# Performance work log

Hardware: AMD Instinct MI355X
Metric: run time of the kernel (lower is better)

## Reference

```python
import jax, jax.numpy as jnp
import numpy as np

# DH-SFNN: 2 dendritic LIF layers (denri, no tanh, reset-by-subtraction) + leaky readout integrator.
GAMMA = 0.5   # surrogate gradient scale
LENS = 0.5    # surrogate gradient width
VTH = 1.0     # spike threshold
DT = 1.0

@jax.custom_vjp
def spike_fn(x):
    # Heaviside forward, Gaussian surrogate backward (act_fun_adp)
    return (x > 0.0).astype(x.dtype)

def _spike_fwd(x):
    return spike_fn(x), x

def _spike_bwd(x, g):
    sg = GAMMA * jnp.exp(-x * x / (2.0 * LENS * LENS)) / (jnp.sqrt(2.0 * jnp.pi) * LENS)
    return (g * sg,)

spike_fn.defvjp(_spike_fwd, _spike_bwd)

B, T, IN, H, O, K = 256, 250, 700, 256, 20, 4  # batch, time, in_dim, hidden, out_dim, branch
WARMUP = 10


def _branch_mask(rng, out_dim, in_dim, k):
    # Each neuron's k branches see a disjoint random partition of the inputs.
    m = np.zeros((out_dim * k, in_dim), np.float32)
    step = in_dim // k
    for i in range(out_dim):
        perm = rng.permutation(in_dim)
        for j in range(k):
            m[i * k + j, perm[j * step:(j + 1) * step]] = 1.0
    return m


def setup_inputs() -> dict:
    key = jax.random.key(0)
    ks = jax.random.split(key, 12)
    rng = np.random.default_rng(0)
    s1 = 1.0 / np.sqrt(IN)
    s2 = 1.0 / np.sqrt(H)
    # branch-masked dense weights (apply_mask() already baked in)
    W1 = jax.random.uniform(ks[0], (H * K, IN), minval=-s1, maxval=s1) * jnp.asarray(_branch_mask(rng, H, IN, K))
    b1 = jax.random.uniform(ks[1], (H * K,), minval=-s1, maxval=s1)
    tau_n1 = jax.random.uniform(ks[2], (H, K), minval=2.0, maxval=6.0)
    tau_m1 = jax.random.uniform(ks[3], (H,), minval=0.0, maxval=4.0)
    W2 = jax.random.uniform(ks[4], (H * K, H), minval=-s2, maxval=s2) * jnp.asarray(_branch_mask(rng, H, H, K))
    b2 = jax.random.uniform(ks[5], (H * K,), minval=-s2, maxval=s2)
    tau_n2 = jax.random.uniform(ks[6], (H, K), minval=2.0, maxval=6.0)
    tau_m2 = jax.random.uniform(ks[7], (H,), minval=0.0, maxval=4.0)
    Wr = jax.random.uniform(ks[8], (O, H), minval=-s2, maxval=s2)
    br = jax.random.uniform(ks[9], (O,), minval=-s2, maxval=s2)
    tau_mr = jax.random.uniform(ks[10], (O,), minval=0.0, maxval=4.0)
    # sparse binary spike train input (SHD-like)
    x = (jax.random.uniform(ks[11], (B, T, IN)) < 0.1).astype(jnp.float32)
    return dict(x=x, W1=W1, b1=b1, tau_n1=tau_n1, tau_m1=tau_m1,
                W2=W2, b2=b2, tau_n2=tau_n2, tau_m2=tau_m2,
                Wr=Wr, br=br, tau_mr=tau_mr, warmup=WARMUP)


def reference(x, W1, b1, tau_n1, tau_m1, W2, b2, tau_n2, tau_m2, Wr, br, tau_mr, warmup):
    Bb, Tt, _ = x.shape
    beta1 = jax.nn.sigmoid(tau_n1)   # [H,K] dendritic decay
    alpha1 = jax.nn.sigmoid(tau_m1)  # [H]   soma decay
    beta2 = jax.nn.sigmoid(tau_n2)
    alpha2 = jax.nn.sigmoid(tau_m2)
    alphar = jax.nn.sigmoid(tau_mr)  # [O]

    def dense_branch(inp, W, b):
        return (inp @ W.T + b).reshape(inp.shape[0], -1, K)  # [B,H,K]

    def step(carry, xt):
        d1, m1, s1, d2, m2, s2, mr, acc, t = carry
        # layer 1: dendritic filtering then LIF with soft reset
        d1 = beta1 * d1 + (1.0 - beta1) * dense_branch(xt, W1, b1)
        m1 = m1 * alpha1 + (1.0 - alpha1) * DT * d1.sum(-1) - VTH * s1
        s1 = spike_fn(m1 - VTH)
        # layer 2
        d2 = beta2 * d2 + (1.0 - beta2) * dense_branch(s1, W2, b2)
        m2 = m2 * alpha2 + (1.0 - alpha2) * DT * d2.sum(-1) - VTH * s2
        s2 = spike_fn(m2 - VTH)
        # leaky readout integrator
        mr = mr * alphar + (1.0 - alphar) * (s2 @ Wr.T + br)
        acc = acc + jnp.where(t >= warmup, mr, jnp.zeros_like(mr))
        return (d1, m1, s1, d2, m2, s2, mr, acc, t + 1), None

    z = lambda *s: jnp.zeros(s, x.dtype)
    carry0 = (z(Bb, H, K), z(Bb, H), z(Bb, H),
              z(Bb, H, K), z(Bb, H), z(Bb, H),
              z(Bb, O), z(Bb, O), jnp.int32(0))
    carry, _ = jax.lax.scan(step, carry0, jnp.moveaxis(x, 1, 0))
    acc = carry[7]
    return acc / (Tt - warmup)  # readout_mode == 'mean'
```

## Files before the change

kernel.cpp:

```cpp
#include <hip/hip_runtime.h>
#include <hip/hip_bf16.h>

typedef unsigned short us16;
typedef unsigned int u32;

#define B_   256
#define T_   250
#define IN_  700
#define KP_  704
#define H_   256
#define O_   20
#define HK_  1024
#define NPAIR_ (B_ * T_)
#define LDP_ 40
#define CP_  132

typedef __attribute__((ext_vector_type(8))) short short8;
typedef __attribute__((ext_vector_type(4))) float f32x4;

__device__ __forceinline__ float bfbits(unsigned int lo16) {
    union { unsigned int i; float f; } v; v.i = lo16 << 16; return v.f;
}
__device__ __forceinline__ float bflo(unsigned int u) {
    union { unsigned int i; float f; } v; v.i = u << 16; return v.f;
}
__device__ __forceinline__ float bfhi(unsigned int u) {
    union { unsigned int i; float f; } v; v.i = u & 0xffff0000u; return v.f;
}
__device__ __forceinline__ us16 f2bfu(float f) {
    __hip_bfloat16 h = __float2bfloat16(f);
    union { __hip_bfloat16 h; us16 u; } c; c.h = h; return c.u;
}
__device__ __forceinline__ float sigm(float x) { return 1.0f / (1.0f + expf(-x)); }
__device__ __forceinline__ int rfl(int v) { return __builtin_amdgcn_readfirstlane(v); }

__device__ __forceinline__ bool detect_bf16(const us16* __restrict__ taun) {
    int ok = 0;
#pragma unroll
    for (int i = 0; i < 8; i += 2) ok += ((taun[i] >> 8) == 0x40) ? 1 : 0;
    return ok == 4;
}
__device__ __forceinline__ float ldany(const void* __restrict__ p, long i, bool isb) {
    return isb ? bfbits(((const us16*)p)[i]) : ((const float*)p)[i];
}

__device__ __forceinline__ void async_cp16(const us16* g, us16* l) {
    __builtin_amdgcn_global_load_lds(
        (const __attribute__((address_space(1))) u32*)g,
        (__attribute__((address_space(3))) u32*)l, 16, 0, 0);
}

__global__ __launch_bounds__(256) void cvt_rows(
    const void* __restrict__ in, us16* __restrict__ out,
    int R, const us16* __restrict__ taun) {
    const bool isb = detect_bf16(taun);
    const int r = blockIdx.x * 4 + (threadIdx.x >> 6);
    const int l = threadIdx.x & 63;
    if (r >= R) return;
    const long ibase = (long)r * IN_;
    const long obase = (long)r * KP_;
    for (int c = l; c < 176; c += 64) {
        uint2 o;
        if (c < 175) {
            if (isb) {
                o = *(const uint2*)((const us16*)in + ibase + 4 * c);
            } else {
                float4 f = *(const float4*)((const float*)in + ibase + 4 * c);
                o.x = (u32)f2bfu(f.x) | ((u32)f2bfu(f.y) << 16);
                o.y = (u32)f2bfu(f.z) | ((u32)f2bfu(f.w) << 16);
            }
        } else { o.x = 0u; o.y = 0u; }
        *(uint2*)(out + obase + 4 * c) = o;
    }
}

__global__ void transpose_to_bf16(const void* __restrict__ in, us16* __restrict__ out,
                                  int R, int C, const us16* __restrict__ taun) {
    const bool isb = detect_bf16(taun);
    __shared__ us16 tile[32][33];
    int c0 = blockIdx.x * 32, r0 = blockIdx.y * 32;
    int tx = threadIdx.x, ty = threadIdx.y;
#pragma unroll
    for (int j = 0; j < 32; j += 8) {
        int r = r0 + ty + j, c = c0 + tx;
        if (r < R && c < C) tile[ty + j][tx] = f2bfu(ldany(in, (long)r * C + c, isb));
    }
    __syncthreads();
#pragma unroll
    for (int j = 0; j < 32; j += 8) {
        int c = c0 + ty + j, r = r0 + tx;
        if (c < C && r < R) out[(long)c * R + r] = tile[tx][ty + j];
    }
}

__global__ __launch_bounds__(256) void gemm_bf(
    const us16* __restrict__ Xb, const us16* __restrict__ W1b,
    us16* __restrict__ Apre)
{
    __shared__ __align__(16) us16 smem[128 * CP_];
    us16* As = smem;
    us16* Bs = smem + 128 * 64;

    const int L  = blockIdx.x;
    const int mt = (L & 7) + ((L >> 6) << 3);
    const int nt = (L >> 3) & 7;
    if (mt >= NPAIR_ / 128) return;
    const int m0 = mt * 128, n0 = nt * 128;

    const int tid  = threadIdx.x;
    const int lane = tid & 63;
    const int w    = tid >> 6;
    const int wr   = w >> 1, wc = w & 1;
    const int l16  = lane & 15, quad = lane >> 4;

    const int rr    = lane >> 3;
    const int ccsw  = ((lane & 7) ^ rr) * 8;
    const us16* xg[4]; const us16* wg[4];
    us16* asl[4]; us16* bsl[4];
#pragma unroll
    for (int i = 0; i < 4; ++i) {
        const int blkrow = (w * 4 + i) * 8;
        xg[i]  = Xb  + (long)(m0 + blkrow + rr) * KP_ + ccsw;
        wg[i]  = W1b + (long)(n0 + blkrow + rr) * KP_ + ccsw;
        asl[i] = As + (w * 4 + i) * 512;
        bsl[i] = Bs + (w * 4 + i) * 512;
    }

    f32x4 acc[4][4];
#pragma unroll
    for (int i = 0; i < 4; ++i)
#pragma unroll
        for (int j = 0; j < 4; ++j) acc[i][j] = (f32x4){0.f, 0.f, 0.f, 0.f};

    const int sw = l16 & 7;
    int aoff0[4], aoff1[4], boff0[4], boff1[4];
#pragma unroll
    for (int i = 0; i < 4; ++i) {
        const int ar = wr * 64 + i * 16 + l16;
        const int br = wc * 64 + i * 16 + l16;
        aoff0[i] = ar * 64 + ((quad ^ sw) << 3);
        aoff1[i] = ar * 64 + (((quad + 4) ^ sw) << 3);
        boff0[i] = br * 64 + ((quad ^ sw) << 3);
        boff1[i] = br * 64 + (((quad + 4) ^ sw) << 3);
    }

    for (int s = 0; s < 11; ++s) {
        const int kb = s * 64;
        __syncthreads();
#pragma unroll
        for (int i = 0; i < 4; ++i) async_cp16(xg[i] + kb, asl[i]);
#pragma unroll
        for (int i = 0; i < 4; ++i) async_cp16(wg[i] + kb, bsl[i]);
        __syncthreads();

        short8 af[4][2], bfv[4][2];
#pragma unroll
        for (int i = 0; i < 4; ++i) {
            af[i][0]  = *(const short8*)(As + aoff0[i]);
            af[i][1]  = *(const short8*)(As + aoff1[i]);
            bfv[i][0] = *(const short8*)(Bs + boff0[i]);
            bfv[i][1] = *(const short8*)(Bs + boff1[i]);
        }
#pragma unroll
        for (int h = 0; h < 2; ++h)
#pragma unroll
            for (int i = 0; i < 4; ++i)
#pragma unroll
                for (int j = 0; j < 4; ++j)
                    acc[i][j] = __builtin_amdgcn_mfma_f32_16x16x32_bf16(
                        af[i][h], bfv[j][h], acc[i][j], 0, 0, 0);
    }

    __syncthreads();
#pragma unroll
    for (int i = 0; i < 4; ++i)
#pragma unroll
        for (int j = 0; j < 4; ++j)
#pragma unroll
            for (int r = 0; r < 4; ++r)
                smem[(wr * 64 + i * 16 + quad * 4 + r) * CP_ +
                     (wc * 64 + j * 16 + l16)] = f2bfu(acc[i][j][r]);
    __syncthreads();
    for (int r2 = 0; r2 < 32; ++r2) {
        const int row = w * 32 + r2;
        const u32 v = *(const u32*)(smem + row * CP_ + lane * 2);
        *(u32*)(Apre + (long)(m0 + row) * HK_ + n0 + lane * 2) = v;
    }
}

__global__ __launch_bounds__(256) void dhsfnn_pc(
    const us16* __restrict__ Apre,
    const void* __restrict__ b1,  const void* __restrict__ tau_n1,
    const void* __restrict__ tau_m1,
    const void* __restrict__ b2,  const void* __restrict__ tau_n2,
    const void* __restrict__ tau_m2,
    const void* __restrict__ Wr,  const void* __restrict__ br,
    const void* __restrict__ tau_mr,
    const us16* __restrict__ W2T,
    const int* __restrict__ warmup_p,
    void* __restrict__ out)
{
    __shared__ __align__(16) us16 ring[2][16 * HK_];

    const int tid  = threadIdx.x;
    const int lane = tid & 63;
    const int w    = tid >> 6;
    const int b    = blockIdx.x;
    const bool isb = detect_bf16((const us16*)tau_n1);
    const int wu   = *warmup_p;

    const us16* apb = Apre + (long)b * T_ * HK_;

    {
        const uint4* src = (const uint4*)apb;
        uint4* dst = (uint4*)ring[0];
        for (int k = tid; k < 16 * 128; k += 256) dst[k] = src[k];
    }

    float be1[16], cb1[16], ce1[16], be2[16], cb2[16], ce2[16], d1[16], d2[16];
#pragma unroll
    for (int e = 0; e < 16; ++e) {
        const long gi = (e < 8) ? ((long)lane * 8 + e) : (512 + (long)lane * 8 + e - 8);
        const float t1 = sigm(ldany(tau_n1, gi, isb));
        be1[e] = t1; ce1[e] = 1.f - t1; cb1[e] = ce1[e] * ldany(b1, gi, isb);
        const float t2 = sigm(ldany(tau_n2, gi, isb));
        be2[e] = t2; ce2[e] = 1.f - t2; cb2[e] = ce2[e] * ldany(b2, gi, isb);
        d1[e] = 0.f; d2[e] = 0.f;
    }
    float al1[4], al2[4], m1[4], s1[4], m2[4], s2[4];
#pragma unroll
    for (int j = 0; j < 4; ++j) {
        const int n = (j < 2) ? (2 * lane + j) : (128 + 2 * lane + (j - 2));
        al1[j] = sigm(ldany(tau_m1, n, isb));
        al2[j] = sigm(ldany(tau_m2, n, isb));
        m1[j] = 0.f; s1[j] = 0.f; m2[j] = 0.f; s2[j] = 0.f;
    }
    float alr = 0.f, brv = 0.f;
    if (lane < O_) { alr = sigm(ldany(tau_mr, lane, isb)); brv = ldany(br, lane, isb); }
    float mrv = 0.f, accO = 0.f;

    __syncthreads();

    for (int c = 0; c < 16; ++c) {
        const int t0 = c * 16;
        const int nst = (T_ - t0 < 16) ? (T_ - t0) : 16;

        if (w != 0) {
            if (c + 1 < 16) {
                const int t1c = (c + 1) * 16;
                const int nn  = ((T_ - t1c < 16) ? (T_ - t1c) : 16) * 128;
                const uint4* src = (const uint4*)(apb + (long)t1c * HK_);
                uint4* dst = (uint4*)ring[(c + 1) & 1];
                for (int k = tid - 64; k < nn; k += 192) dst[k] = src[k];
            }
        } else {
            const us16* rb = ring[c & 1];
            uint4 cLo = *(const uint4*)(rb + lane * 8);
            uint4 cHi = *(const uint4*)(rb + 512 + lane * 8);
            for (int q = 0; q < nst; ++q) {
                uint4 nLo = cLo, nHi = cHi;
                if (q + 1 < nst) {
                    nLo = *(const uint4*)(rb + (q + 1) * HK_ + lane * 8);
                    nHi = *(const uint4*)(rb + (q + 1) * HK_ + 512 + lane * 8);
                }
                const int t = t0 + q;
                float a[16];
                a[0]=bflo(cLo.x);  a[1]=bfhi(cLo.x);  a[2]=bflo(cLo.y);  a[3]=bfhi(cLo.y);
                a[4]=bflo(cLo.z);  a[5]=bfhi(cLo.z);  a[6]=bflo(cLo.w);  a[7]=bfhi(cLo.w);
                a[8]=bflo(cHi.x);  a[9]=bfhi(cHi.x);  a[10]=bflo(cHi.y); a[11]=bfhi(cHi.y);
                a[12]=bflo(cHi.z); a[13]=bfhi(cHi.z); a[14]=bflo(cHi.w); a[15]=bfhi(cHi.w);

#pragma unroll
                for (int e = 0; e < 16; ++e)
                    d1[e] = be1[e] * d1[e] + cb1[e] + ce1[e] * a[e];

                unsigned long long bal1[4];
#pragma unroll
                for (int j = 0; j < 4; ++j) {
                    const float s = (d1[j*4+0] + d1[j*4+1]) + (d1[j*4+2] + d1[j*4+3]);
                    m1[j] = m1[j] * al1[j] + (1.f - al1[j]) * s - s1[j];
                    s1[j] = (m1[j] > 1.0f) ? 1.f : 0.f;
                    bal1[j] = __ballot(s1[j] > 0.f);
                }

                if ((bal1[0] | bal1[1] | bal1[2] | bal1[3]) != 0ull) {
                    float g[16];
#pragma unroll
                    for (int e = 0; e < 16; ++e) g[e] = 0.f;
                    for (int j2 = 0; j2 < 4; ++j2) {
                        unsigned long long mm = bal1[j2];
                        while (mm) {
                            const int i = __ffsll(mm) - 1; mm &= mm - 1;
                            const int n = (j2 < 2) ? (2 * i + j2) : (128 + 2 * i + (j2 - 2));
                            const us16* wv = W2T + ((long)n << 10);
                            const uint4 wl = *(const uint4*)(wv + lane * 8);
                            const uint4 wh = *(const uint4*)(wv + 512 + lane * 8);
                            g[0]+=bflo(wl.x);  g[1]+=bfhi(wl.x);  g[2]+=bflo(wl.y);  g[3]+=bfhi(wl.y);
                            g[4]+=bflo(wl.z);  g[5]+=bfhi(wl.z);  g[6]+=bflo(wl.w);  g[7]+=bfhi(wl.w);
                            g[8]+=bflo(wh.x);  g[9]+=bfhi(wh.x);  g[10]+=bflo(wh.y); g[11]+=bfhi(wh.y);
                            g[12]+=bflo(wh.z); g[13]+=bfhi(wh.z); g[14]+=bflo(wh.w); g[15]+=bfhi(wh.w);
                        }
                    }
#pragma unroll
                    for (int e = 0; e < 16; ++e)
                        d2[e] = be2[e] * d2[e] + cb2[e] + ce2[e] * g[e];
                } else {
#pragma unroll
                    for (int e = 0; e < 16; ++e)
                        d2[e] = be2[e] * d2[e] + cb2[e];
                }

                unsigned long long bal2[4];
#pragma unroll
                for (int j = 0; j < 4; ++j) {
                    const float s = (d2[j*4+0] + d2[j*4+1]) + (d2[j*4+2] + d2[j*4+3]);
                    m2[j] = m2[j] * al2[j] + (1.f - al2[j]) * s - s2[j];
                    s2[j] = (m2[j] > 1.0f) ? 1.f : 0.f;
                    bal2[j] = __ballot(s2[j] > 0.f);
                }

                if (lane < O_) {
                    float sum = brv;
                    if ((bal2[0] | bal2[1] | bal2[2] | bal2[3]) != 0ull) {
                        for (int j2 = 0; j2 < 4; ++j2) {
                            unsigned long long mm = bal2[j2];
                            while (mm) {
                                const int i = __ffsll(mm) - 1; mm &= mm - 1;
                                const int n = (j2 < 2) ? (2 * i + j2) : (128 + 2 * i + (j2 - 2));
                                sum += ldany(Wr, (long)lane * H_ + n, isb);
                            }
                        }
                    }
                    mrv = alr * mrv + (1.f - alr) * sum;
                    if (t >= wu) accO += mrv;
                }
                cLo = nLo; cHi = nHi;
            }
        }
        __syncthreads();
    }

    if (w == 0 && lane < O_) {
        const float res = accO / (float)(T_ - wu);
        if (isb) ((us16*)out)[b * O_ + lane] = f2bfu(res);
        else     ((float*)out)[b * O_ + lane] = res;
    }
}

#define GA_LOAD(S, AV, BV) do {                                               \
    const int k0_ = (S) * 32 + half16;                                        \
    if (k0_ + 16 <= IN_) {                                                    \
        if (isb) {                                                            \
            const us16* pa_ = (const us16*)X  + arow + k0_;                   \
            const us16* pb_ = (const us16*)W1 + brow + k0_;                   \
            uint2 a0_ = *(const uint2*)pa_,        a1_ = *(const uint2*)(pa_ + 4);  \
            uint2 a2_ = *(const uint2*)(pa_ + 8),  a3_ = *(const uint2*)(pa_ + 12); \
            uint2 b0_ = *(const uint2*)pb_,        b1_ = *(const uint2*)(pb_ + 4);  \
            uint2 b2_ = *(const uint2*)(pb_ + 8),  b3_ = *(const uint2*)(pb_ + 12); \
            AV[0]=a0_.x; AV[1]=a0_.y; AV[2]=a1_.x; AV[3]=a1_.y;               \
            AV[4]=a2_.x; AV[5]=a2_.y; AV[6]=a3_.x; AV[7]=a3_.y;               \
            BV[0]=b0_.x; BV[1]=b0_.y; BV[2]=b1_.x; BV[3]=b1_.y;               \
            BV[4]=b2_.x; BV[5]=b2_.y; BV[6]=b3_.x; BV[7]=b3_.y;               \
        } else {                                                              \
            const float* pa_ = (const float*)X  + arow + k0_;                 \
            const float* pb_ = (const float*)W1 + brow + k0_;                 \
            float4 fa0_ = *(const float4*)pa_,        fa1_ = *(const float4*)(pa_ + 4);  \
            float4 fa2_ = *(const float4*)(pa_ + 8),  fa3_ = *(const float4*)(pa_ + 12); \
            float4 fb0_ = *(const float4*)pb_,        fb1_ = *(const float4*)(pb_ + 4);  \
            float4 fb2_ = *(const float4*)(pb_ + 8),  fb3_ = *(const float4*)(pb_ + 12); \
            AV[0] = (unsigned)f2bfu(fa0_.x) | ((unsigned)f2bfu(fa0_.y) << 16); \
            AV[1] = (unsigned)f2bfu(fa0_.z) | ((unsigned)f2bfu(fa0_.w) << 16); \
            AV[2] = (unsigned)f2bfu(fa1_.x) | ((unsigned)f2bfu(fa1_.y) << 16); \
            AV[3] = (unsigned)f2bfu(fa1_.z) | ((unsigned)f2bfu(fa1_.w) << 16); \
            AV[4] = (unsigned)f2bfu(fa2_.x) | ((unsigned)f2bfu(fa2_.y) << 16); \
            AV[5] = (unsigned)f2bfu(fa2_.z) | ((unsigned)f2bfu(fa2_.w) << 16); \
            AV[6] = (unsigned)f2bfu(fa3_.x) | ((unsigned)f2bfu(fa3_.y) << 16); \
            AV[7] = (unsigned)f2bfu(fa3_.z) | ((unsigned)f2bfu(fa3_.w) << 16); \
            BV[0] = (unsigned)f2bfu(fb0_.x) | ((unsigned)f2bfu(fb0_.y) << 16); \
            BV[1] = (unsigned)f2bfu(fb0_.z) | ((unsigned)f2bfu(fb0_.w) << 16); \
            BV[2] = (unsigned)f2bfu(fb1_.x) | ((unsigned)f2bfu(fb1_.y) << 16); \
            BV[3] = (unsigned)f2bfu(fb1_.z) | ((unsigned)f2bfu(fb1_.w) << 16); \
            BV[4] = (unsigned)f2bfu(fb2_.x) | ((unsigned)f2bfu(fb2_.y) << 16); \
            BV[5] = (unsigned)f2bfu(fb2_.z) | ((unsigned)f2bfu(fb2_.w) << 16); \
            BV[6] = (unsigned)f2bfu(fb3_.x) | ((unsigned)f2bfu(fb3_.y) << 16); \
            BV[7] = (unsigned)f2bfu(fb3_.z) | ((unsigned)f2bfu(fb3_.w) << 16); \
        }                                                                     \
    } else {                                                                  \
        _Pragma("unroll")                                                     \
        for (int e_ = 0; e_ < 8; ++e_) { AV[e_] = 0u; BV[e_] = 0u; }          \
        _Pragma("unroll")                                                     \
        for (int e_ = 0; e_ < 16; ++e_) {                                     \
            int k_ = k0_ + e_;                                                \
            if (k_ < IN_) {                                                   \
                unsigned va_ = (unsigned)f2bfu(ldany(X,  arow + k_, isb));    \
                unsigned vb_ = (unsigned)f2bfu(ldany(W1, brow + k_, isb));    \
                AV[e_ >> 1] |= va_ << ((e_ & 1) * 16);                        \
                BV[e_ >> 1] |= vb_ << ((e_ & 1) * 16);                        \
            }                                                                 \
        }                                                                     \
    }                                                                         \
} while (0)

#define GA_STORE(AV, BV) do {                                                 \
    uint4 u0_; u0_.x = AV[0]; u0_.y = AV[1]; u0_.z = AV[2]; u0_.w = AV[3];    \
    uint4 u1_; u1_.x = AV[4]; u1_.y = AV[5]; u1_.z = AV[6]; u1_.w = AV[7];    \
    uint4 v0_; v0_.x = BV[0]; v0_.y = BV[1]; v0_.z = BV[2]; v0_.w = BV[3];    \
    uint4 v1_; v1_.x = BV[4]; v1_.y = BV[5]; v1_.z = BV[6]; v1_.w = BV[7];    \
    *(uint4*)asw       = u0_; *(uint4*)(asw + 8) = u1_;                       \
    *(uint4*)bsw       = v0_; *(uint4*)(bsw + 8) = v1_;                       \
} while (0)

#define GA_MFMA() do {                                                        \
    short8 af_[4], bf_[4];                                                    \
    _Pragma("unroll")                                                         \
    for (int i_ = 0; i_ < 4; ++i_) af_[i_] = *(const short8*)(As + aoff[i_]); \
    _Pragma("unroll")                                                         \
    for (int j_ = 0; j_ < 4; ++j_) bf_[j_] = *(const short8*)(Bs + boff[j_]); \
    _Pragma("unroll")                                                         \
    for (int i_ = 0; i_ < 4; ++i_)                                            \
        _Pragma("unroll")                                                     \
        for (int j_ = 0; j_ < 4; ++j_)                                        \
            acc[i_][j_] = __builtin_amdgcn_mfma_f32_16x16x32_bf16(            \
                af_[i_], bf_[j_], acc[i_][j_], 0, 0, 0);                      \
} while (0)

__global__ __launch_bounds__(256) void gemm_apre(
    const void* __restrict__ X, const void* __restrict__ W1,
    const us16* __restrict__ taun, us16* __restrict__ Apre)
{
    const bool isb = detect_bf16(taun);
    __shared__ __align__(16) us16 As[128 * LDP_];
    __shared__ __align__(16) us16 Bs[128 * LDP_];

    const int L  = blockIdx.x;
    const int mt = (L & 7) + ((L >> 6) << 3);
    const int nt = (L >> 3) & 7;
    if (mt >= NPAIR_ / 128) return;
    const int m0 = mt * 128, n0 = nt * 128;

    const int tid  = threadIdx.x;
    const int lane = tid & 63;
    const int w    = tid >> 6;
    const int wr   = w >> 1, wc = w & 1;
    const int l16  = lane & 15, quad = lane >> 4;
    const int ra   = tid >> 1;
    const int half16 = (tid & 1) * 16;

    f32x4 acc[4][4];
#pragma unroll
    for (int i = 0; i < 4; ++i)
#pragma unroll
        for (int j = 0; j < 4; ++j) acc[i][j] = (f32x4){0.f, 0.f, 0.f, 0.f};

    int aoff[4], boff[4];
#pragma unroll
    for (int i = 0; i < 4; ++i) {
        aoff[i] = (wr * 64 + i * 16 + l16) * LDP_ + quad * 8;
        boff[i] = (wc * 64 + i * 16 + l16) * LDP_ + quad * 8;
    }

    const long arow = (long)(m0 + ra) * IN_;
    const long brow = (long)(n0 + ra) * IN_;
    us16* asw = As + ra * LDP_ + half16;
    us16* bsw = Bs + ra * LDP_ + half16;

    unsigned av0[8], bv0[8], av1[8], bv1[8];
    GA_LOAD(0, av0, bv0);

    for (int ss = 0; ss < 11; ++ss) {
        __syncthreads();
        GA_STORE(av0, bv0);
        __syncthreads();
        GA_LOAD(2 * ss + 1, av1, bv1);
        GA_MFMA();
        __syncthreads();
        GA_STORE(av1, bv1);
        __syncthreads();
        if (ss < 10) GA_LOAD(2 * ss + 2, av0, bv0);
        GA_MFMA();
    }

#pragma unroll
    for (int i = 0; i < 4; ++i) {
#pragma unroll
        for (int j = 0; j < 4; ++j) {
            const int gm = m0 + wr * 64 + i * 16 + quad * 4;
            const int gn = n0 + wc * 64 + j * 16 + l16;
            us16* op = Apre + (long)gm * HK_ + gn;
#pragma unroll
            for (int r = 0; r < 4; ++r)
                op[(long)r * HK_] = f2bfu(acc[i][j][r]);
        }
    }
}

__global__ __launch_bounds__(64) void dhsfnn_wave(
    const us16* __restrict__ Apre,
    const void* __restrict__ b1,  const void* __restrict__ tau_n1,
    const void* __restrict__ tau_m1,
    const void* __restrict__ b2,  const void* __restrict__ tau_n2,
    const void* __restrict__ tau_m2,
    const void* __restrict__ Wr,  const void* __restrict__ br,
    const void* __restrict__ tau_mr,
    const us16* __restrict__ W2T,
    const int* __restrict__ warmup_p,
    void* __restrict__ out)
{
    const int lane = threadIdx.x;
    const int b    = blockIdx.x;
    const bool isb = detect_bf16((const us16*)tau_n1);
    const int wu   = *warmup_p;

    float be1[16], cb1[16], be2[16], cb2[16], d1[16], d2[16];
#pragma unroll
    for (int e = 0; e < 16; ++e) {
        const long gi = (long)lane * 16 + e;
        const float t1 = sigm(ldany(tau_n1, gi, isb));
        be1[e] = t1; cb1[e] = (1.f - t1) * ldany(b1, gi, isb);
        const float t2 = sigm(ldany(tau_n2, gi, isb));
        be2[e] = t2; cb2[e] = (1.f - t2) * ldany(b2, gi, isb);
        d1[e] = 0.f; d2[e] = 0.f;
    }
    float al1[4], al2[4], m1[4], s1[4], m2[4], s2[4];
#pragma unroll
    for (int j = 0; j < 4; ++j) {
        al1[j] = sigm(ldany(tau_m1, lane * 4 + j, isb));
        al2[j] = sigm(ldany(tau_m2, lane * 4 + j, isb));
        m1[j] = 0.f; s1[j] = 0.f; m2[j] = 0.f; s2[j] = 0.f;
    }
    float alr = 0.f, brv = 0.f;
    if (lane < O_) { alr = sigm(ldany(tau_mr, lane, isb)); brv = ldany(br, lane, isb); }
    float mrv = 0.f, accO = 0.f;

    const us16* ap = Apre + (long)b * T_ * HK_ + lane * 16;

    auto wstep = [&](int t, uint4 lo, uint4 hi) {
        float a[16];
        a[0]=bflo(lo.x);  a[1]=bfhi(lo.x);  a[2]=bflo(lo.y);  a[3]=bfhi(lo.y);
        a[4]=bflo(lo.z);  a[5]=bfhi(lo.z);  a[6]=bflo(lo.w);  a[7]=bfhi(lo.w);
        a[8]=bflo(hi.x);  a[9]=bfhi(hi.x);  a[10]=bflo(hi.y); a[11]=bfhi(hi.y);
        a[12]=bflo(hi.z); a[13]=bfhi(hi.z); a[14]=bflo(hi.w); a[15]=bfhi(hi.w);
#pragma unroll
        for (int e = 0; e < 16; ++e)
            d1[e] = be1[e] * d1[e] + cb1[e] + (1.f - be1[e]) * a[e];
        unsigned long long bal1[4];
#pragma unroll
        for (int j = 0; j < 4; ++j) {
            const float s = (d1[j*4+0] + d1[j*4+1]) + (d1[j*4+2] + d1[j*4+3]);
            m1[j] = m1[j] * al1[j] + (1.f - al1[j]) * s - s1[j];
            s1[j] = (m1[j] > 1.0f) ? 1.f : 0.f;
            bal1[j] = __ballot(s1[j] > 0.f);
        }
        if ((bal1[0] | bal1[1] | bal1[2] | bal1[3]) != 0ull) {
            float g[16];
#pragma unroll
            for (int e = 0; e < 16; ++e) g[e] = 0.f;
            for (int j2 = 0; j2 < 4; ++j2) {
                unsigned long long mm = bal1[j2];
                while (mm) {
                    const int i = __ffsll(mm) - 1; mm &= mm - 1;
                    const us16* wv = W2T + ((long)(i * 4 + j2) << 10) + lane * 16;
                    const uint4 wl = *(const uint4*)wv;
                    const uint4 wh = *(const uint4*)(wv + 8);
                    g[0]+=bflo(wl.x);  g[1]+=bfhi(wl.x);  g[2]+=bflo(wl.y);  g[3]+=bfhi(wl.y);
                    g[4]+=bflo(wl.z);  g[5]+=bfhi(wl.z);  g[6]+=bflo(wl.w);  g[7]+=bfhi(wl.w);
                    g[8]+=bflo(wh.x);  g[9]+=bfhi(wh.x);  g[10]+=bflo(wh.y); g[11]+=bfhi(wh.y);
                    g[12]+=bflo(wh.z); g[13]+=bfhi(wh.z); g[14]+=bflo(wh.w); g[15]+=bfhi(wh.w);
                }
            }
#pragma unroll
            for (int e = 0; e < 16; ++e)
                d2[e] = be2[e] * d2[e] + cb2[e] + (1.f - be2[e]) * g[e];
        } else {
#pragma unroll
            for (int e = 0; e < 16; ++e)
                d2[e] = be2[e] * d2[e] + cb2[e];
        }
        unsigned long long bal2[4];
#pragma unroll
        for (int j = 0; j < 4; ++j) {
            const float s = (d2[j*4+0] + d2[j*4+1]) + (d2[j*4+2] + d2[j*4+3]);
            m2[j] = m2[j] * al2[j] + (1.f - al2[j]) * s - s2[j];
            s2[j] = (m2[j] > 1.0f) ? 1.f : 0.f;
            bal2[j] = __ballot(s2[j] > 0.f);
        }
        if (lane < O_) {
            float sum = brv;
            if ((bal2[0] | bal2[1] | bal2[2] | bal2[3]) != 0ull) {
                for (int j2 = 0; j2 < 4; ++j2) {
                    unsigned long long mm = bal2[j2];
                    while (mm) {
                        const int i = __ffsll(mm) - 1; mm &= mm - 1;
                        sum += ldany(Wr, (long)lane * H_ + (i * 4 + j2), isb);
                    }
                }
            }
            mrv = alr * mrv + (1.f - alr) * sum;
            if (t >= wu) accO += mrv;
        }
    };

    uint4 q0a = *(const uint4*)(ap);
    uint4 q0b = *(const uint4*)(ap + 8);
    uint4 q1a = *(const uint4*)(ap + HK_);
    uint4 q1b = *(const uint4*)(ap + HK_ + 8);
    uint4 q2a = *(const uint4*)(ap + 2 * HK_);
    uint4 q2b = *(const uint4*)(ap + 2 * HK_ + 8);
    uint4 q3a = *(const uint4*)(ap + 3 * HK_);
    uint4 q3b = *(const uint4*)(ap + 3 * HK_ + 8);

    int t = 0;
    for (int it = 0; it < 62; ++it) {
        wstep(t + 0, q0a, q0b);
        q0a = *(const uint4*)(ap + (long)(t + 4) * HK_);
        q0b = *(const uint4*)(ap + (long)(t + 4) * HK_ + 8);
        wstep(t + 1, q1a, q1b);
        if (t + 5 < T_) {
            q1a = *(const uint4*)(ap + (long)(t + 5) * HK_);
            q1b = *(const uint4*)(ap + (long)(t + 5) * HK_ + 8);
        }
        wstep(t + 2, q2a, q2b);
        if (t + 6 < T_) {
            q2a = *(const uint4*)(ap + (long)(t + 6) * HK_);
            q2b = *(const uint4*)(ap + (long)(t + 6) * HK_ + 8);
        }
        wstep(t + 3, q3a, q3b);
        if (t + 7 < T_) {
            q3a = *(const uint4*)(ap + (long)(t + 7) * HK_);
            q3b = *(const uint4*)(ap + (long)(t + 7) * HK_ + 8);
        }
        t += 4;
    }
    wstep(248, q0a, q0b);
    wstep(249, q1a, q1b);

    if (lane < O_) {
        const float res = accO / (float)(T_ - wu);
        if (isb) ((us16*)out)[b * O_ + lane] = f2bfu(res);
        else     ((float*)out)[b * O_ + lane] = res;
    }
}

__global__ __launch_bounds__(256) void dhsfnn_fb(
    const void* __restrict__ x,  const void* __restrict__ W1,
    const void* __restrict__ b1, const void* __restrict__ tau_n1,
    const void* __restrict__ tau_m1,
    const void* __restrict__ W2, const void* __restrict__ b2,
    const void* __restrict__ tau_n2, const void* __restrict__ tau_m2,
    const void* __restrict__ Wr, const void* __restrict__ br,
    const void* __restrict__ tau_mr,
    const int* __restrict__ warmup_p,
    void* __restrict__ out)
{
    __shared__ us16 list1[1024];
    __shared__ us16 list2[256];
    __shared__ us16 list3[256];
    __shared__ int n1s, n2s, n3s;

    const int tid = threadIdx.x;
    const int b   = blockIdx.x;
    const int h   = tid;
    const bool isb = detect_bf16((const us16*)tau_n1);
    const int wu  = *warmup_p;

    const float be1_0 = sigm(ldany(tau_n1, 4 * h + 0, isb));
    const float be1_1 = sigm(ldany(tau_n1, 4 * h + 1, isb));
    const float be1_2 = sigm(ldany(tau_n1, 4 * h + 2, isb));
    const float be1_3 = sigm(ldany(tau_n1, 4 * h + 3, isb));
    const float bi1_0 = ldany(b1, 4 * h + 0, isb), bi1_1 = ldany(b1, 4 * h + 1, isb);
    const float bi1_2 = ldany(b1, 4 * h + 2, isb), bi1_3 = ldany(b1, 4 * h + 3, isb);
    const float al1 = sigm(ldany(tau_m1, h, isb));
    const float be2_0 = sigm(ldany(tau_n2, 4 * h + 0, isb));
    const float be2_1 = sigm(ldany(tau_n2, 4 * h + 1, isb));
    const float be2_2 = sigm(ldany(tau_n2, 4 * h + 2, isb));
    const float be2_3 = sigm(ldany(tau_n2, 4 * h + 3, isb));
    const float bi2_0 = ldany(b2, 4 * h + 0, isb), bi2_1 = ldany(b2, 4 * h + 1, isb);
    const float bi2_2 = ldany(b2, 4 * h + 2, isb), bi2_3 = ldany(b2, 4 * h + 3, isb);
    const float al2 = sigm(ldany(tau_m2, h, isb));
    float alr = 0.f, brv = 0.f;
    if (h < O_) { alr = sigm(ldany(tau_mr, h, isb)); brv = ldany(br, h, isb); }

    float d1_0 = 0.f, d1_1 = 0.f, d1_2 = 0.f, d1_3 = 0.f, m1v = 0.f, s1f = 0.f;
    float d2_0 = 0.f, d2_1 = 0.f, d2_2 = 0.f, d2_3 = 0.f, m2v = 0.f, s2f = 0.f;
    float mrv = 0.f, accO = 0.f;

    const long xbase = (long)b * T_ * IN_;
    float xv0 = ldany(x, xbase + tid, isb);
    float xv1 = ldany(x, xbase + tid + 256, isb);
    float xv2 = (tid + 512 < IN_) ? ldany(x, xbase + tid + 512, isb) : 0.f;

    for (int t = 0; t < T_; ++t) {
        const bool p0 = xv0 != 0.f, p1 = xv1 != 0.f, p2 = xv2 != 0.f;
        if (t + 1 < T_) {
            const long nbx = xbase + (long)(t + 1) * IN_;
            xv0 = ldany(x, nbx + tid, isb);
            xv1 = ldany(x, nbx + tid + 256, isb);
            xv2 = (tid + 512 < IN_) ? ldany(x, nbx + tid + 512, isb) : 0.f;
        }
        __syncthreads();
        if (tid == 0) { n1s = 0; n2s = 0; n3s = 0; }
        __syncthreads();
        if (p0) { int p = atomicAdd(&n1s, 1); list1[p & 1023] = (us16)tid; }
        if (p1) { int p = atomicAdd(&n1s, 1); list1[p & 1023] = (us16)(tid + 256); }
        if (p2) { int p = atomicAdd(&n1s, 1); list1[p & 1023] = (us16)(tid + 512); }
        __syncthreads();
        int n1 = n1s; n1 = (n1 < 1024) ? n1 : 1024;

        float a0 = 0.f, a1 = 0.f, a2 = 0.f, a3 = 0.f;
#pragma unroll 2
        for (int idx = 0; idx < n1; ++idx) {
            int i = rfl((int)list1[idx]);
            i = (i < IN_) ? i : (IN_ - 1);
            long r = (long)(h * 4) * IN_ + i;
            a0 += ldany(W1, r, isb);
            a1 += ldany(W1, r + IN_, isb);
            a2 += ldany(W1, r + 2 * IN_, isb);
            a3 += ldany(W1, r + 3 * IN_, isb);
        }
        d1_0 = be1_0 * d1_0 + (1.f - be1_0) * (bi1_0 + a0);
        d1_1 = be1_1 * d1_1 + (1.f - be1_1) * (bi1_1 + a1);
        d1_2 = be1_2 * d1_2 + (1.f - be1_2) * (bi1_2 + a2);
        d1_3 = be1_3 * d1_3 + (1.f - be1_3) * (bi1_3 + a3);
        m1v = m1v * al1 + (1.f - al1) * (d1_0 + d1_1 + d1_2 + d1_3) - s1f;
        s1f = (m1v > 1.0f) ? 1.f : 0.f;

        if (s1f > 0.f) { int p = atomicAdd(&n2s, 1); list2[p & 255] = (us16)tid; }
        __syncthreads();
        int n2 = n2s; n2 = (n2 < 256) ? n2 : 256;

        a0 = 0.f; a1 = 0.f; a2 = 0.f; a3 = 0.f;
#pragma unroll 2
        for (int idx = 0; idx < n2; ++idx) {
            int i = rfl((int)list2[idx]);
            i = (i < H_) ? i : (H_ - 1);
            long r = (long)(h * 4) * H_ + i;
            a0 += ldany(W2, r, isb);
            a1 += ldany(W2, r + H_, isb);
            a2 += ldany(W2, r + 2 * H_, isb);
            a3 += ldany(W2, r + 3 * H_, isb);
        }
        d2_0 = be2_0 * d2_0 + (1.f - be2_0) * (bi2_0 + a0);
        d2_1 = be2_1 * d2_1 + (1.f - be2_1) * (bi2_1 + a1);
        d2_2 = be2_2 * d2_2 + (1.f - be2_2) * (bi2_2 + a2);
        d2_3 = be2_3 * d2_3 + (1.f - be2_3) * (bi2_3 + a3);
        m2v = m2v * al2 + (1.f - al2) * (d2_0 + d2_1 + d2_2 + d2_3) - s2f;
        s2f = (m2v > 1.0f) ? 1.f : 0.f;

        if (s2f > 0.f) { int p = atomicAdd(&n3s, 1); list3[p & 255] = (us16)tid; }
        __syncthreads();
        int n3 = n3s; n3 = (n3 < 256) ? n3 : 256;

        if (h < O_) {
            float sum = brv;
            for (int idx = 0; idx < n3; ++idx) {
                int j = (int)list3[idx];
                j = (j < H_) ? j : (H_ - 1);
                sum += ldany(Wr, (long)h * H_ + j, isb);
            }
            mrv = alr * mrv + (1.f - alr) * sum;
            if (t >= wu) accO += mrv;
        }
    }
    if (h < O_) {
        float res = accO / (float)(T_ - wu);
        if (isb) ((us16*)out)[b * O_ + h] = f2bfu(res);
        else     ((float*)out)[b * O_ + h] = res;
    }
}

extern "C" void kernel_launch(void* const* d_in, const int* in_sizes, int n_in,
                              void* d_out, int out_size, void* d_ws, size_t ws_size,
                              hipStream_t stream) {
    const void* x      = d_in[0];
    const void* W1     = d_in[1];
    const void* b1     = d_in[2];
    const void* tau_n1 = d_in[3];
    const void* tau_m1 = d_in[4];
    const void* W2     = d_in[5];
    const void* b2     = d_in[6];
    const void* tau_n2 = d_in[7];
    const void* tau_m2 = d_in[8];
    const void* Wr     = d_in[9];
    const void* br     = d_in[10];
    const void* tau_mr = d_in[11];
    const int*  warmup = (const int*)d_in[12];

    const size_t w2t_bytes  = (size_t)H_ * HK_ * 2;
    const size_t xbf_bytes  = (size_t)NPAIR_ * KP_ * 2;
    const size_t w1b_bytes  = (size_t)HK_ * KP_ * 2;
    const size_t apre_bytes = (size_t)NPAIR_ * HK_ * 2;

    const bool tier0 = (d_ws != nullptr &&
                        ws_size >= w2t_bytes + xbf_bytes + w1b_bytes + apre_bytes);
    const bool tier1 = (d_ws != nullptr && ws_size >= w2t_bytes + apre_bytes);

    dim3 blk(32, 8);
    if (tier0) {
        us16* W2T  = (us16*)d_ws;
        us16* Xbf  = (us16*)((char*)d_ws + w2t_bytes);
        us16* W1bf = (us16*)((char*)d_ws + w2t_bytes + xbf_bytes);
        us16* Apre = (us16*)((char*)d_ws + w2t_bytes + xbf_bytes + w1b_bytes);
        cvt_rows<<<NPAIR_ / 4, 256, 0, stream>>>(x, Xbf, NPAIR_, (const us16*)tau_n1);
        cvt_rows<<<HK_ / 4, 256, 0, stream>>>(W1, W1bf, HK_, (const us16*)tau_n1);
        transpose_to_bf16<<<dim3((H_ + 31) / 32, (HK_ + 31) / 32), blk, 0, stream>>>(
            W2, W2T, HK_, H_, (const us16*)tau_n1);
        gemm_bf<<<4096, 256, 0, stream>>>(Xbf, W1bf, Apre);
        dhsfnn_pc<<<B_, 256, 0, stream>>>(
            Apre, b1, tau_n1, tau_m1, b2, tau_n2, tau_m2,
            Wr, br, tau_mr, W2T, warmup, d_out);
    } else if (tier1) {
        us16* W2T  = (us16*)d_ws;
        us16* Apre = (us16*)((char*)d_ws + w2t_bytes);
        transpose_to_bf16<<<dim3((H_ + 31) / 32, (HK_ + 31) / 32), blk, 0, stream>>>(
            W2, W2T, HK_, H_, (const us16*)tau_n1);
        gemm_apre<<<4096, 256, 0, stream>>>(x, W1, (const us16*)tau_n1, Apre);
        dhsfnn_wave<<<B_, 64, 0, stream>>>(
            Apre, b1, tau_n1, tau_m1, b2, tau_n2, tau_m2,
            Wr, br, tau_mr, W2T, warmup, d_out);
    } else {
        dhsfnn_fb<<<B_, 256, 0, stream>>>(x, W1, b1, tau_n1, tau_m1,
                                          W2, b2, tau_n2, tau_m2,
                                          Wr, br, tau_mr, warmup, d_out);
    }
}
```

Before: 481.7 us.

## Enlarge GEMM M-tile to 256 rows and merge input conversion kernels

The bf16 GEMM for the layer-1 pre-activations now computes 256x128 tiles instead of 128x128, halving the grid and reusing each loaded W1 slice across twice as many rows. The epilogue writes the result through shared memory in two passes. The separate x and W1 conversion launches are merged into one kernel to save a launch. The change raises accumulator register pressure (32 f32x4 per thread), which may lower occupancy.

```diff
diff --git a/kernel.cpp b/kernel.cpp
--- a/kernel.cpp
+++ b/kernel.cpp
@@ -50,15 +50,21 @@
         (__attribute__((address_space(3))) u32*)l, 16, 0, 0);
 }
 
-__global__ __launch_bounds__(256) void cvt_rows(
-    const void* __restrict__ in, us16* __restrict__ out,
-    int R, const us16* __restrict__ taun) {
+__global__ __launch_bounds__(256) void cvt_rows2(
+    const void* __restrict__ xin, const void* __restrict__ w1in,
+    us16* __restrict__ xout, us16* __restrict__ w1out,
+    const us16* __restrict__ taun) {
     const bool isb = detect_bf16(taun);
     const int r = blockIdx.x * 4 + (threadIdx.x >> 6);
     const int l = threadIdx.x & 63;
-    if (r >= R) return;
-    const long ibase = (long)r * IN_;
-    const long obase = (long)r * KP_;
+    const void* in; us16* out; long ibase, obase;
+    if (r < NPAIR_) {
+        in = xin;  out = xout;  ibase = (long)r * IN_; obase = (long)r * KP_;
+    } else {
+        const int r2 = r - NPAIR_;
+        if (r2 >= HK_) return;
+        in = w1in; out = w1out; ibase = (long)r2 * IN_; obase = (long)r2 * KP_;
+    }
     for (int c = l; c < 176; c += 64) {
         uint2 o;
         if (c < 175) {
@@ -97,15 +103,15 @@
     const us16* __restrict__ Xb, const us16* __restrict__ W1b,
     us16* __restrict__ Apre)
 {
-    __shared__ __align__(16) us16 smem[128 * CP_];
+    __shared__ __align__(16) us16 smem[24576];
     us16* As = smem;
-    us16* Bs = smem + 128 * 64;
+    us16* Bs = smem + 16384;
 
     const int L  = blockIdx.x;
     const int mt = (L & 7) + ((L >> 6) << 3);
     const int nt = (L >> 3) & 7;
-    if (mt >= NPAIR_ / 128) return;
-    const int m0 = mt * 128, n0 = nt * 128;
+    if (mt >= NPAIR_ / 256) return;
+    const int m0 = mt * 256, n0 = nt * 128;
 
     const int tid  = threadIdx.x;
     const int lane = tid & 63;
@@ -113,78 +119,91 @@
     const int wr   = w >> 1, wc = w & 1;
     const int l16  = lane & 15, quad = lane >> 4;
 
-    const int rr    = lane >> 3;
-    const int ccsw  = ((lane & 7) ^ rr) * 8;
-    const us16* xg[4]; const us16* wg[4];
-    us16* asl[4]; us16* bsl[4];
+    const int rr   = lane >> 3;
+    const int ccsw = ((lane & 7) ^ rr) * 8;
+    const us16* xg[8]; us16* asl[8];
+    const us16* wg[4]; us16* bsl[4];
+#pragma unroll
+    for (int i = 0; i < 8; ++i) {
+        const int g = w * 8 + i;
+        xg[i]  = Xb + (long)(m0 + g * 8 + rr) * KP_ + ccsw;
+        asl[i] = As + g * 512;
+    }
 #pragma unroll
     for (int i = 0; i < 4; ++i) {
-        const int blkrow = (w * 4 + i) * 8;
-        xg[i]  = Xb  + (long)(m0 + blkrow + rr) * KP_ + ccsw;
-        wg[i]  = W1b + (long)(n0 + blkrow + rr) * KP_ + ccsw;
-        asl[i] = As + (w * 4 + i) * 512;
-        bsl[i] = Bs + (w * 4 + i) * 512;
-    }
-
-    f32x4 acc[4][4];
-#pragma unroll
-    for (int i = 0; i < 4; ++i)
+        const int g = w * 4 + i;
+        wg[i]  = W1b + (long)(n0 + g * 8 + rr) * KP_ + ccsw;
+        bsl[i] = Bs + g * 512;
+    }
+
+    f32x4 acc[8][4];
+#pragma unroll
+    for (int i = 0; i < 8; ++i)
 #pragma unroll
         for (int j = 0; j < 4; ++j) acc[i][j] = (f32x4){0.f, 0.f, 0.f, 0.f};
 
     const int sw = l16 & 7;
-    int aoff0[4], aoff1[4], boff0[4], boff1[4];
-#pragma unroll
-    for (int i = 0; i < 4; ++i) {
-        const int ar = wr * 64 + i * 16 + l16;
-        const int br = wc * 64 + i * 16 + l16;
+    int aoff0[8], aoff1[8], boff0[4], boff1[4];
+#pragma unroll
+    for (int i = 0; i < 8; ++i) {
+        const int ar = wr * 128 + i * 16 + l16;
         aoff0[i] = ar * 64 + ((quad ^ sw) << 3);
         aoff1[i] = ar * 64 + (((quad + 4) ^ sw) << 3);
-        boff0[i] = br * 64 + ((quad ^ sw) << 3);
-        boff1[i] = br * 64 + (((quad + 4) ^ sw) << 3);
+    }
+#pragma unroll
+    for (int j = 0; j < 4; ++j) {
+        const int br = wc * 64 + j * 16 + l16;
+        boff0[j] = br * 64 + ((quad ^ sw) << 3);
+        boff1[j] = br * 64 + (((quad + 4) ^ sw) << 3);
     }
 
     for (int s = 0; s < 11; ++s) {
         const int kb = s * 64;
         __syncthreads();
 #pragma unroll
-        for (int i = 0; i < 4; ++i) async_cp16(xg[i] + kb, asl[i]);
+        for (int i = 0; i < 8; ++i) async_cp16(xg[i] + kb, asl[i]);
 #pragma unroll
         for (int i = 0; i < 4; ++i) async_cp16(wg[i] + kb, bsl[i]);
         __syncthreads();
 
-        short8 af[4][2], bfv[4][2];
-#pragma unroll
-        for (int i = 0; i < 4; ++i) {
-            af[i][0]  = *(const short8*)(As + aoff0[i]);
-            af[i][1]  = *(const short8*)(As + aoff1[i]);
-            bfv[i][0] = *(const short8*)(Bs + boff0[i]);
-            bfv[i][1] = *(const short8*)(Bs + boff1[i]);
-        }
-#pragma unroll
-        for (int h = 0; h < 2; ++h)
-#pragma unroll
-            for (int i = 0; i < 4; ++i)
+        short8 bfv[4][2];
+#pragma unroll
+        for (int j = 0; j < 4; ++j) {
+            bfv[j][0] = *(const short8*)(Bs + boff0[j]);
+            bfv[j][1] = *(const short8*)(Bs + boff1[j]);
+        }
+#pragma unroll
+        for (int i = 0; i < 8; ++i) {
+            const short8 a0 = *(const short8*)(As + aoff0[i]);
+            const short8 a1 = *(const short8*)(As + aoff1[i]);
+#pragma unroll
+            for (int j = 0; j < 4; ++j) {
+                acc[i][j] = __builtin_amdgcn_mfma_f32_16x16x32_bf16(
+                    a0, bfv[j][0], acc[i][j], 0, 0, 0);
+                acc[i][j] = __builtin_amdgcn_mfma_f32_16x16x32_bf16(
+                    a1, bfv[j][1], acc[i][j], 0, 0, 0);
+            }
+        }
+    }
+
+    for (int p = 0; p < 2; ++p) {
+        __syncthreads();
+        if (wr == p) {
+#pragma unroll
+            for (int i = 0; i < 8; ++i)
 #pragma unroll
                 for (int j = 0; j < 4; ++j)
-                    acc[i][j] = __builtin_amdgcn_mfma_f32_16x16x32_bf16(
-                        af[i][h], bfv[j][h], acc[i][j], 0, 0, 0);
-    }
-
-    __syncthreads();
-#pragma unroll
-    for (int i = 0; i < 4; ++i)
-#pragma unroll
-        for (int j = 0; j < 4; ++j)
-#pragma unroll
-            for (int r = 0; r < 4; ++r)
-                smem[(wr * 64 + i * 16 + quad * 4 + r) * CP_ +
-                     (wc * 64 + j * 16 + l16)] = f2bfu(acc[i][j][r]);
-    __syncthreads();
-    for (int r2 = 0; r2 < 32; ++r2) {
-        const int row = w * 32 + r2;
-        const u32 v = *(const u32*)(smem + row * CP_ + lane * 2);
-        *(u32*)(Apre + (long)(m0 + row) * HK_ + n0 + lane * 2) = v;
+#pragma unroll
+                    for (int r = 0; r < 4; ++r)
+                        smem[(i * 16 + quad * 4 + r) * CP_ +
+                             (wc * 64 + j * 16 + l16)] = f2bfu(acc[i][j][r]);
+        }
+        __syncthreads();
+        for (int r2 = 0; r2 < 32; ++r2) {
+            const int row = w * 32 + r2;
+            const u32 v = *(const u32*)(smem + row * CP_ + lane * 2);
+            *(u32*)(Apre + (long)(m0 + p * 128 + row) * HK_ + n0 + lane * 2) = v;
+        }
     }
 }
 
@@ -800,11 +819,11 @@
         us16* Xbf  = (us16*)((char*)d_ws + w2t_bytes);
         us16* W1bf = (us16*)((char*)d_ws + w2t_bytes + xbf_bytes);
         us16* Apre = (us16*)((char*)d_ws + w2t_bytes + xbf_bytes + w1b_bytes);
-        cvt_rows<<<NPAIR_ / 4, 256, 0, stream>>>(x, Xbf, NPAIR_, (const us16*)tau_n1);
-        cvt_rows<<<HK_ / 4, 256, 0, stream>>>(W1, W1bf, HK_, (const us16*)tau_n1);
+        cvt_rows2<<<(NPAIR_ + HK_) / 4, 256, 0, stream>>>(
+            x, W1, Xbf, W1bf, (const us16*)tau_n1);
         transpose_to_bf16<<<dim3((H_ + 31) / 32, (HK_ + 31) / 32), blk, 0, stream>>>(
             W2, W2T, HK_, H_, (const us16*)tau_n1);
-        gemm_bf<<<4096, 256, 0, stream>>>(Xbf, W1bf, Apre);
+        gemm_bf<<<2048, 256, 0, stream>>>(Xbf, W1bf, Apre);
         dhsfnn_pc<<<B_, 256, 0, stream>>>(
             Apre, b1, tau_n1, tau_m1, b2, tau_n2, tau_m2,
             Wr, br, tau_mr, W2T, warmup, d_out);
```

Result: slower. 552.8 us (+14.8%).
